# Kernel optimization log

Measured on AMD Instinct MI355X. Metric: run time of the kernel, lower is better.

## Reference

```python
import jax, jax.numpy as jnp
import numpy as np

GAMMA = 1.0  # init arg gamma


def setup_inputs() -> dict:
    key = jax.random.key(0)
    ks = jax.random.split(key, 7)
    Bn, C, C_, H = 8, 256, 32, 64
    sc = 1.0 / np.sqrt(C)
    return {
        "x_activation": jax.random.normal(ks[0], (Bn, C, H, H), dtype=jnp.float32),
        "f_w": jax.random.normal(ks[1], (C_, C), dtype=jnp.float32) * sc,
        "f_b": jnp.zeros((C_,), dtype=jnp.float32),
        "g_w": jax.random.normal(ks[2], (C_, C), dtype=jnp.float32) * sc,
        "g_b": jnp.zeros((C_,), dtype=jnp.float32),
        "h_w": jax.random.normal(ks[3], (C, C), dtype=jnp.float32) * sc,
        "h_b": jnp.zeros((C,), dtype=jnp.float32),
    }


def reference(x_activation, f_w, f_b, g_w, g_b, h_w, h_b):
    Bn, C, H, W = x_activation.shape
    N = H * W
    xf = x_activation.reshape(Bn, C, N)  # [B, C, N]
    # 1x1 convs are per-pixel linear maps over channels
    f = jnp.einsum('oc,bcn->bon', f_w, xf) + f_b[:, None]  # [B, C_, N]
    g = jnp.einsum('oc,bcn->bon', g_w, xf) + g_b[:, None]  # [B, C_, N]
    h = jnp.einsum('oc,bcn->bon', h_w, xf) + h_b[:, None]  # [B, C, N]
    # S[b, i, j] = sum_c f[b, c, i] * g[b, c, j]  (f^T @ g), shape [B, N, N]
    S = jnp.einsum('bci,bcj->bij', f, g)
    # NOTE: original uses Softmax(dim=1) -> normalize over the i (query/f) axis
    B = jax.nn.softmax(S, axis=1)
    # O (post-transpose) [b, c, i] = sum_j B[b, i, j] * h[b, c, j]
    O = jnp.einsum('bij,bcj->bci', B, h).reshape(Bn, C, H, W)
    return GAMMA * O + x_activation
```

## Files before the change

kernel.cpp:

```cpp
#include <hip/hip_runtime.h>
#include <hip/hip_fp16.h>
#include <cmath>


#define BN 8
#define CC 256
#define CQ 32
#define NN 4096

typedef _Float16 half8 __attribute__((ext_vector_type(8)));
typedef _Float16 half4v __attribute__((ext_vector_type(4)));
typedef float f32x4 __attribute__((ext_vector_type(4)));

static __device__ __forceinline__ float fexp2(float x) {
    return __builtin_amdgcn_exp2f(x);
}

#define LOG2E 1.44269504f
#define SHIFT2 28.8539008f

__global__ __launch_bounds__(256) void cvtw_kernel(
    const float* __restrict__ fw, const float* __restrict__ gw,
    const float* __restrict__ hw, __half* __restrict__ wf16)
{
    int i = blockIdx.x * 256 + threadIdx.x;
    float v;
    if (i < 8192)       v = fw[i];
    else if (i < 16384) v = gw[i - 8192];
    else                v = hw[i - 16384];
    wf16[i] = __float2half(v);
}

__global__ __launch_bounds__(256) void transpose_kernel(
    const float* __restrict__ x, __half* __restrict__ xt)
{
    const int gid = blockIdx.x;
    const int b = gid & 7, rest = gid >> 3;
    const int n0 = (rest & 63) * 64;
    const int c0 = (rest >> 6) * 64;
    const int tid = threadIdx.x;

    __shared__ float T[64 * 65];

    const float* xb = x + ((size_t)b * CC + c0) * NN + n0;
    const int u  = tid >> 4;
    const int n4 = (tid & 15) * 4;
#pragma unroll
    for (int r = 0; r < 4; ++r) {
        int c = r * 16 + u;
        f32x4 v = __builtin_nontemporal_load((const f32x4*)(xb + (size_t)c * NN + n4));
        T[c * 65 + n4 + 0] = v.x;
        T[c * 65 + n4 + 1] = v.y;
        T[c * 65 + n4 + 2] = v.z;
        T[c * 65 + n4 + 3] = v.w;
    }
    __syncthreads();

    const int lane = tid & 63, w = tid >> 6;
    const int n  = w * 16 + (lane >> 2);
    const int cc = (lane & 3) * 16;
    half8 o0, o1;
#pragma unroll
    for (int k = 0; k < 8; ++k) {
        o0[k] = (_Float16)T[(cc + k) * 65 + n];
        o1[k] = (_Float16)T[(cc + 8 + k) * 65 + n];
    }
    __half* dst = xt + ((size_t)b * NN + n0 + n) * CC + c0 + cc;
    *(half8*)(void*)dst = o0;
    *(half8*)(void*)(dst + 8) = o1;
}

__global__ __launch_bounds__(256) void proj_kernel(
    const __half* __restrict__ xt, const __half* __restrict__ wf16,
    const float* __restrict__ fb, const float* __restrict__ gb,
    const float* __restrict__ hb,
    __half* __restrict__ ft, __half* __restrict__ gt, __half* __restrict__ hm)
{
    const int tid = threadIdx.x;
    const int w = tid >> 6, lane = tid & 63, col = lane & 15, q = lane >> 4;
    const int gid = blockIdx.x;
    const int b = gid & 7, rest = gid >> 3;
    const int n0 = (rest & 63) * 64;
    const int ot = rest >> 6;

    const __half* xtb  = xt + (size_t)b * NN * CC;
    const __half* fw16 = wf16;
    const __half* gw16 = wf16 + 8192;
    const __half* hw16 = wf16 + 16384;

    f32x4 acc[4];
#pragma unroll
    for (int mt = 0; mt < 4; ++mt) acc[mt] = (f32x4){0.f, 0.f, 0.f, 0.f};

    if (ot == 0) {
        const int pix = n0 + 16 * w + col;
#pragma unroll
        for (int ks = 0; ks < 8; ++ks) {
            half8 bf = *(const half8*)(const void*)(xtb + (size_t)pix * CC + ks * 32 + q * 8);
#pragma unroll
            for (int mt = 0; mt < 4; ++mt) {
                const __half* wp = (mt < 2) ? (fw16 + (16 * mt + col) * CC)
                                            : (gw16 + (16 * (mt - 2) + col) * CC);
                half8 af = *(const half8*)(const void*)(wp + ks * 32 + q * 8);
                acc[mt] = __builtin_amdgcn_mfma_f32_16x16x32_f16(af, bf, acc[mt], 0, 0, 0);
            }
        }
#pragma unroll
        for (int mt = 0; mt < 4; ++mt) {
            const int mtl = mt & 1;
            const float* bsel = (mt < 2) ? fb : gb;
            __half* dsel = (mt < 2) ? ft : gt;
            half4v hv;
#pragma unroll
            for (int r = 0; r < 4; ++r)
                hv[r] = (_Float16)(acc[mt][r] + bsel[16 * mtl + 4 * q + r]);
            *(half4v*)(void*)(dsel + ((size_t)b * NN + pix) * CQ + 16 * mtl + 4 * q) = hv;
        }
    } else {
        const int c = (ot - 1) * 64 + 16 * w + col;
#pragma unroll
        for (int ks = 0; ks < 8; ++ks) {
            half8 bf = *(const half8*)(const void*)(hw16 + (size_t)c * CC + ks * 32 + q * 8);
#pragma unroll
            for (int mt = 0; mt < 4; ++mt) {
                half8 af = *(const half8*)(const void*)(xtb + (size_t)(n0 + 16 * mt + col) * CC + ks * 32 + q * 8);
                acc[mt] = __builtin_amdgcn_mfma_f32_16x16x32_f16(af, bf, acc[mt], 0, 0, 0);
            }
        }
        const float bias = hb[c];
#pragma unroll
        for (int mt = 0; mt < 4; ++mt) {
            half4v hv;
#pragma unroll
            for (int r = 0; r < 4; ++r)
                hv[r] = (_Float16)(acc[mt][r] + bias);
            *(half4v*)(void*)(hm + ((size_t)b * CC + c) * NN + n0 + 16 * mt + 4 * q) = hv;
        }
    }
}

__global__ __launch_bounds__(256) void pass1_kernel(
    const __half* __restrict__ ft, const __half* __restrict__ gt,
    float* __restrict__ linv)
{
    const int tid = threadIdx.x;
    const int w = tid >> 6, lane = tid & 63, col = lane & 15, q = lane >> 4;
    const int gid = blockIdx.x;
    const int b = gid & 7;
    const int jg = (gid >> 3) * 64 + 16 * w + col;

    const __half* fbase = ft + (size_t)b * NN * CQ;
    half8 gfrag = *(const half8*)(const void*)(gt + ((size_t)b * NN + jg) * CQ + q * 8);

    float a0 = 0.f, a1 = 0.f, a2 = 0.f, a3 = 0.f;
    const f32x4 zero = {0.f, 0.f, 0.f, 0.f};

    half8 a_cur = *(const half8*)(const void*)(fbase + (size_t)col * CQ + q * 8);
    for (int i0 = 0; i0 < NN; i0 += 16) {
        int i_n = (i0 + 16) & (NN - 1);
        half8 a_next = *(const half8*)(const void*)(fbase + (size_t)(i_n + col) * CQ + q * 8);
        f32x4 d = __builtin_amdgcn_mfma_f32_16x16x32_f16(a_cur, gfrag, zero, 0, 0, 0);
        a0 += fexp2(fmaf(d[0], LOG2E, -SHIFT2));
        a1 += fexp2(fmaf(d[1], LOG2E, -SHIFT2));
        a2 += fexp2(fmaf(d[2], LOG2E, -SHIFT2));
        a3 += fexp2(fmaf(d[3], LOG2E, -SHIFT2));
        a_cur = a_next;
    }
    float l = (a0 + a1) + (a2 + a3);
    l += __shfl_xor(l, 16);
    l += __shfl_xor(l, 32);
    if (q == 0)
        linv[(size_t)b * NN + jg] = 1.f / l;
}

__global__ __launch_bounds__(256, 4) void pass2_kernel(
    const float* __restrict__ x,
    const __half* __restrict__ ft, const __half* __restrict__ gt,
    const __half* __restrict__ hm, const float* __restrict__ linv,
    float* __restrict__ out)
{
    const int tid = threadIdx.x;
    const int w = tid >> 6, lane = tid & 63, col = lane & 15, q = lane >> 4;
    const int gid = blockIdx.x;
    const int b  = gid & 7;
    const int r2 = gid >> 3;
    const int i0 = (r2 & 63) * 64;
    const int cb = (r2 >> 6) * 128 + 32 * w;

    __shared__ __half P[2][64 * 64];

    const __half* gbase = gt + (size_t)b * NN * CQ;
    const __half* hbase = hm + (size_t)b * CC * NN;
    const float*  lb    = linv + (size_t)b * NN;

    half8 ffr[4];
#pragma unroll
    for (int it = 0; it < 4; ++it)
        ffr[it] = *(const half8*)(const void*)(ft + ((size_t)b * NN + i0 + 16 * it + col) * CQ + q * 8);

    f32x4 acc[4][2];
#pragma unroll
    for (int ms = 0; ms < 4; ++ms)
#pragma unroll
        for (int ns = 0; ns < 2; ++ns)
            acc[ms][ns] = (f32x4){0.f, 0.f, 0.f, 0.f};

    const f32x4 zero = {0.f, 0.f, 0.f, 0.f};
    const int jml = 16 * w + 4 * q;
    const int sw  = 8 * (col & 7);

    half8  gfr = *(const half8*)(const void*)(gbase + (size_t)(16 * w + col) * CQ + q * 8);
    float4 il  = *(const float4*)(lb + jml);

    int buf = 0;
    for (int j0 = 0; j0 < NN; j0 += 64, buf ^= 1) {
        half8 hv[2][2];
#pragma unroll
        for (int ns = 0; ns < 2; ++ns)
#pragma unroll
            for (int ks = 0; ks < 2; ++ks)
                hv[ns][ks] = *(const half8*)(const void*)(
                    hbase + (size_t)(cb + 16 * ns + col) * NN + j0 + ks * 32 + q * 8);

        f32x4 d[4];
#pragma unroll
        for (int it = 0; it < 4; ++it)
            d[it] = __builtin_amdgcn_mfma_f32_16x16x32_f16(gfr, ffr[it], zero, 0, 0, 0);

        const int jn = (j0 + 64) & (NN - 1);
        half8  gfr_n = *(const half8*)(const void*)(gbase + (size_t)(jn + 16 * w + col) * CQ + q * 8);
        float4 il_n  = *(const float4*)(lb + jn + jml);

        __half* Pb = &P[buf][0];
#pragma unroll
        for (int it = 0; it < 4; ++it) {
            half4v pv;
            pv[0] = (_Float16)(fexp2(fmaf(d[it][0], LOG2E, -SHIFT2)) * il.x);
            pv[1] = (_Float16)(fexp2(fmaf(d[it][1], LOG2E, -SHIFT2)) * il.y);
            pv[2] = (_Float16)(fexp2(fmaf(d[it][2], LOG2E, -SHIFT2)) * il.z);
            pv[3] = (_Float16)(fexp2(fmaf(d[it][3], LOG2E, -SHIFT2)) * il.w);
            *(half4v*)(void*)(Pb + (16 * it + col) * 64 + (jml ^ sw)) = pv;
        }
        __syncthreads();

#pragma unroll
        for (int ks = 0; ks < 2; ++ks) {
            half8 af[4];
#pragma unroll
            for (int ms = 0; ms < 4; ++ms)
                af[ms] = *(const half8*)(const void*)(
                    Pb + (16 * ms + col) * 64 + ((ks * 32 + q * 8) ^ sw));
#pragma unroll
            for (int ms = 0; ms < 4; ++ms)
#pragma unroll
                for (int ns = 0; ns < 2; ++ns)
                    acc[ms][ns] = __builtin_amdgcn_mfma_f32_16x16x32_f16(
                        af[ms], hv[ns][ks], acc[ms][ns], 0, 0, 0);
        }
        gfr = gfr_n;
        il  = il_n;
    }

    const float* xb = x + (size_t)b * CC * NN;
    float* ob = out + (size_t)b * CC * NN;
#pragma unroll
    for (int ms = 0; ms < 4; ++ms) {
#pragma unroll
        for (int ns = 0; ns < 2; ++ns) {
            int c  = cb + 16 * ns + col;
            int ii = i0 + 16 * ms + 4 * q;
            size_t off = (size_t)c * NN + ii;
            f32x4 xv = __builtin_nontemporal_load((const f32x4*)(xb + off));
            f32x4 ov;
            ov.x = acc[ms][ns][0] + xv.x;
            ov.y = acc[ms][ns][1] + xv.y;
            ov.z = acc[ms][ns][2] + xv.z;
            ov.w = acc[ms][ns][3] + xv.w;
            __builtin_nontemporal_store(ov, (f32x4*)(ob + off));
        }
    }
}

extern "C" void kernel_launch(void* const* d_in, const int* in_sizes, int n_in,
                              void* d_out, int out_size, void* d_ws, size_t ws_size,
                              hipStream_t stream)
{
    const float* x  = (const float*)d_in[0];
    const float* fw = (const float*)d_in[1];
    const float* fb = (const float*)d_in[2];
    const float* gw = (const float*)d_in[3];
    const float* gb = (const float*)d_in[4];
    const float* hw = (const float*)d_in[5];
    const float* hb = (const float*)d_in[6];
    float* out = (float*)d_out;

    char* ws = (char*)d_ws;
    __half* xt = (__half*)(ws);
    __half* wf = (__half*)(ws + (size_t)16777216);
    __half* ft = (__half*)(ws + (size_t)17039360);
    __half* gt = (__half*)(ws + (size_t)19136512);
    __half* hm = (__half*)(ws + (size_t)21233664);
    float*  lv = (float*) (ws + (size_t)38010880);

    cvtw_kernel<<<dim3(320), dim3(256), 0, stream>>>(fw, gw, hw, wf);
    transpose_kernel<<<dim3(2048), dim3(256), 0, stream>>>(x, xt);
    proj_kernel<<<dim3(2560), dim3(256), 0, stream>>>(xt, wf, fb, gb, hb, ft, gt, hm);
    pass1_kernel<<<dim3(512), dim3(256), 0, stream>>>(ft, gt, lv);
    pass2_kernel<<<dim3(1024), dim3(256), 0, stream>>>(x, ft, gt, hm, lv, out);
}
```

Before: 341.4 us.

## Split pass2 over key halves with atomic accumulation and fold log2e into projection

The pass2 attention-times-values loop is split into two halves over the j (key) axis, doubling the grid, and each half accumulates into the output with float atomics. A separate kernel first copies x into the output to provide the residual, and the occupancy hint rises to 8 blocks per SM. The log2(e) factor is folded into the f projection and the fixed exponent shift is dropped, which saves an FMA per exponential. pass1 is also unrolled by two with independent accumulators. In exchange the change adds an extra read and write of the output, atomic traffic, non-deterministic summation order, and relies on unshifted exponentials staying within float range.

After: 968.8 us. 184% more time.

```diff
diff --git a/kernel.cpp b/kernel.cpp
--- a/kernel.cpp
+++ b/kernel.cpp
@@ -17,7 +17,6 @@
 }
 
 #define LOG2E 1.44269504f
-#define SHIFT2 28.8539008f
 
 __global__ __launch_bounds__(256) void cvtw_kernel(
     const float* __restrict__ fw, const float* __restrict__ gw,
@@ -109,11 +108,12 @@
         for (int mt = 0; mt < 4; ++mt) {
             const int mtl = mt & 1;
             const float* bsel = (mt < 2) ? fb : gb;
+            const float scale = (mt < 2) ? LOG2E : 1.0f;
             __half* dsel = (mt < 2) ? ft : gt;
             half4v hv;
 #pragma unroll
             for (int r = 0; r < 4; ++r)
-                hv[r] = (_Float16)(acc[mt][r] + bsel[16 * mtl + 4 * q + r]);
+                hv[r] = (_Float16)((acc[mt][r] + bsel[16 * mtl + 4 * q + r]) * scale);
             *(half4v*)(void*)(dsel + ((size_t)b * NN + pix) * CQ + 16 * mtl + 4 * q) = hv;
         }
     } else {
@@ -153,28 +153,37 @@
     half8 gfrag = *(const half8*)(const void*)(gt + ((size_t)b * NN + jg) * CQ + q * 8);
 
     float a0 = 0.f, a1 = 0.f, a2 = 0.f, a3 = 0.f;
+    float b0 = 0.f, b1 = 0.f, b2 = 0.f, b3 = 0.f;
     const f32x4 zero = {0.f, 0.f, 0.f, 0.f};
 
-    half8 a_cur = *(const half8*)(const void*)(fbase + (size_t)col * CQ + q * 8);
-    for (int i0 = 0; i0 < NN; i0 += 16) {
-        int i_n = (i0 + 16) & (NN - 1);
-        half8 a_next = *(const half8*)(const void*)(fbase + (size_t)(i_n + col) * CQ + q * 8);
-        f32x4 d = __builtin_amdgcn_mfma_f32_16x16x32_f16(a_cur, gfrag, zero, 0, 0, 0);
-        a0 += fexp2(fmaf(d[0], LOG2E, -SHIFT2));
-        a1 += fexp2(fmaf(d[1], LOG2E, -SHIFT2));
-        a2 += fexp2(fmaf(d[2], LOG2E, -SHIFT2));
-        a3 += fexp2(fmaf(d[3], LOG2E, -SHIFT2));
-        a_cur = a_next;
-    }
-    float l = (a0 + a1) + (a2 + a3);
+    half8 aA = *(const half8*)(const void*)(fbase + (size_t)col * CQ + q * 8);
+    half8 aB = *(const half8*)(const void*)(fbase + (size_t)(16 + col) * CQ + q * 8);
+    for (int i0 = 0; i0 < NN; i0 += 32) {
+        int i_n = (i0 + 32) & (NN - 1);
+        half8 aA2 = *(const half8*)(const void*)(fbase + (size_t)(i_n + col) * CQ + q * 8);
+        half8 aB2 = *(const half8*)(const void*)(fbase + (size_t)(i_n + 16 + col) * CQ + q * 8);
+        f32x4 d0 = __builtin_amdgcn_mfma_f32_16x16x32_f16(aA, gfrag, zero, 0, 0, 0);
+        f32x4 d1 = __builtin_amdgcn_mfma_f32_16x16x32_f16(aB, gfrag, zero, 0, 0, 0);
+        a0 += fexp2(d0[0]); a1 += fexp2(d0[1]); a2 += fexp2(d0[2]); a3 += fexp2(d0[3]);
+        b0 += fexp2(d1[0]); b1 += fexp2(d1[1]); b2 += fexp2(d1[2]); b3 += fexp2(d1[3]);
+        aA = aA2; aB = aB2;
+    }
+    float l = ((a0 + a1) + (a2 + a3)) + ((b0 + b1) + (b2 + b3));
     l += __shfl_xor(l, 16);
     l += __shfl_xor(l, 32);
     if (q == 0)
         linv[(size_t)b * NN + jg] = 1.f / l;
 }
 
-__global__ __launch_bounds__(256, 4) void pass2_kernel(
-    const float* __restrict__ x,
+__global__ __launch_bounds__(256) void initout_kernel(
+    const float* __restrict__ x, float* __restrict__ out)
+{
+    size_t i = ((size_t)blockIdx.x * 256 + threadIdx.x) * 4;
+    f32x4 v = __builtin_nontemporal_load((const f32x4*)(x + i));
+    __builtin_nontemporal_store(v, (f32x4*)(out + i));
+}
+
+__global__ __launch_bounds__(256, 8) void pass2_kernel(
     const __half* __restrict__ ft, const __half* __restrict__ gt,
     const __half* __restrict__ hm, const float* __restrict__ linv,
     float* __restrict__ out)
@@ -185,7 +194,8 @@
     const int b  = gid & 7;
     const int r2 = gid >> 3;
     const int i0 = (r2 & 63) * 64;
-    const int cb = (r2 >> 6) * 128 + 32 * w;
+    const int cb = ((r2 >> 6) & 1) * 128 + 32 * w;
+    const int J  = ((r2 >> 7) & 1) * 2048;
 
     __shared__ __half P[2][64 * 64];
 
@@ -209,11 +219,12 @@
     const int jml = 16 * w + 4 * q;
     const int sw  = 8 * (col & 7);
 
-    half8  gfr = *(const half8*)(const void*)(gbase + (size_t)(16 * w + col) * CQ + q * 8);
-    float4 il  = *(const float4*)(lb + jml);
+    half8  gfr = *(const half8*)(const void*)(gbase + (size_t)(J + 16 * w + col) * CQ + q * 8);
+    float4 il  = *(const float4*)(lb + J + jml);
 
     int buf = 0;
-    for (int j0 = 0; j0 < NN; j0 += 64, buf ^= 1) {
+    for (int jo = 0; jo < 2048; jo += 64, buf ^= 1) {
+        const int j0 = J + jo;
         half8 hv[2][2];
 #pragma unroll
         for (int ns = 0; ns < 2; ++ns)
@@ -227,7 +238,7 @@
         for (int it = 0; it < 4; ++it)
             d[it] = __builtin_amdgcn_mfma_f32_16x16x32_f16(gfr, ffr[it], zero, 0, 0, 0);
 
-        const int jn = (j0 + 64) & (NN - 1);
+        const int jn = J + ((jo + 64) & 2047);
         half8  gfr_n = *(const half8*)(const void*)(gbase + (size_t)(jn + 16 * w + col) * CQ + q * 8);
         float4 il_n  = *(const float4*)(lb + jn + jml);
 
@@ -235,10 +246,10 @@
 #pragma unroll
         for (int it = 0; it < 4; ++it) {
             half4v pv;
-            pv[0] = (_Float16)(fexp2(fmaf(d[it][0], LOG2E, -SHIFT2)) * il.x);
-            pv[1] = (_Float16)(fexp2(fmaf(d[it][1], LOG2E, -SHIFT2)) * il.y);
-            pv[2] = (_Float16)(fexp2(fmaf(d[it][2], LOG2E, -SHIFT2)) * il.z);
-            pv[3] = (_Float16)(fexp2(fmaf(d[it][3], LOG2E, -SHIFT2)) * il.w);
+            pv[0] = (_Float16)(fexp2(d[it][0]) * il.x);
+            pv[1] = (_Float16)(fexp2(d[it][1]) * il.y);
+            pv[2] = (_Float16)(fexp2(d[it][2]) * il.z);
+            pv[3] = (_Float16)(fexp2(d[it][3]) * il.w);
             *(half4v*)(void*)(Pb + (16 * it + col) * 64 + (jml ^ sw)) = pv;
         }
         __syncthreads();
@@ -261,7 +272,6 @@
         il  = il_n;
     }
 
-    const float* xb = x + (size_t)b * CC * NN;
     float* ob = out + (size_t)b * CC * NN;
 #pragma unroll
     for (int ms = 0; ms < 4; ++ms) {
@@ -269,14 +279,11 @@
         for (int ns = 0; ns < 2; ++ns) {
             int c  = cb + 16 * ns + col;
             int ii = i0 + 16 * ms + 4 * q;
-            size_t off = (size_t)c * NN + ii;
-            f32x4 xv = __builtin_nontemporal_load((const f32x4*)(xb + off));
-            f32x4 ov;
-            ov.x = acc[ms][ns][0] + xv.x;
-            ov.y = acc[ms][ns][1] + xv.y;
-            ov.z = acc[ms][ns][2] + xv.z;
-            ov.w = acc[ms][ns][3] + xv.w;
-            __builtin_nontemporal_store(ov, (f32x4*)(ob + off));
+            float* p = ob + (size_t)c * NN + ii;
+            unsafeAtomicAdd(p + 0, acc[ms][ns][0]);
+            unsafeAtomicAdd(p + 1, acc[ms][ns][1]);
+            unsafeAtomicAdd(p + 2, acc[ms][ns][2]);
+            unsafeAtomicAdd(p + 3, acc[ms][ns][3]);
         }
     }
 }
@@ -306,5 +313,6 @@
     transpose_kernel<<<dim3(2048), dim3(256), 0, stream>>>(x, xt);
     proj_kernel<<<dim3(2560), dim3(256), 0, stream>>>(xt, wf, fb, gb, hb, ft, gt, hm);
     pass1_kernel<<<dim3(512), dim3(256), 0, stream>>>(ft, gt, lv);
-    pass2_kernel<<<dim3(1024), dim3(256), 0, stream>>>(x, ft, gt, hm, lv, out);
-}
+    initout_kernel<<<dim3(8192), dim3(256), 0, stream>>>(x, out);
+    pass2_kernel<<<dim3(2048), dim3(256), 0, stream>>>(ft, gt, hm, lv, out);
+}
```
